# Kernel optimization log

Hardware: AMD Instinct MI355X
Metric: run time of the kernel (lower is better)

## Reference

```python
import jax, jax.numpy as jnp
import numpy as np

N = 20000      # nodes
E = 320000     # edges per metapath graph
M = 3          # metapaths
IN = 256       # input feat dim
HID = 64       # num_hidden per head
NH = 4         # nhead (layer 1)
OUT = 256      # out_dim
NHO = 1        # nhead_out (layer 2)
SA_H = 128     # semantic attention hidden
NEG_SLOPE = 0.2


def gat_conv(h, W, attn_l, attn_r, src, dst, apply_relu):
    # h: [N, F_in]; W: [F_in, H*D]; attn_l/attn_r: [H, D]
    H, D = attn_l.shape
    feat = (h @ W).reshape(N, H, D)                      # [N, H, D]
    el = jnp.sum(feat * attn_l, axis=-1)                 # [N, H]
    er = jnp.sum(feat * attn_r, axis=-1)                 # [N, H]
    e = jax.nn.leaky_relu(el[src] + er[dst], NEG_SLOPE)  # [E, H]
    # edge softmax grouped by destination node
    emax = jax.ops.segment_max(e, dst, num_segments=N)   # [N, H] (-inf for empty)
    emax = jnp.where(jnp.isfinite(emax), emax, 0.0)
    ee = jnp.exp(e - emax[dst])                          # [E, H]
    denom = jax.ops.segment_sum(ee, dst, num_segments=N) # [N, H]
    alpha = ee / (denom[dst] + 1e-9)                     # [E, H]
    msg = alpha[:, :, None] * feat[src]                  # [E, H, D]
    out = jax.ops.segment_sum(msg, dst, num_segments=N)  # [N, H, D]
    out = out.reshape(N, H * D)                          # concat heads
    return jax.nn.relu(out) if apply_relu else out


def semantic_attention(z, W1, b1, v):
    # z: [N, M, F]
    w = jnp.tanh(z @ W1 + b1) @ v          # [N, M, 1]
    w = w.mean(axis=0)                     # [M, 1]
    beta = jax.nn.softmax(w, axis=0)       # [M, 1]
    out = jnp.sum(beta[None, :, :] * z, axis=1)  # [N, F]
    att_mp = beta.squeeze()                # [M]
    return out, att_mp


def setup_inputs() -> dict:
    key = jax.random.key(0)
    ks = jax.random.split(key, 16)
    s = 0.05
    return {
        "x": jax.random.normal(ks[0], (N, IN), dtype=jnp.float32),
        "edges": jax.random.randint(ks[1], (M, 2, E), 0, N, dtype=jnp.int64)
                 if jax.config.jax_enable_x64 else
                 jax.random.randint(ks[1], (M, 2, E), 0, N, dtype=jnp.int32),
        "W1": jax.random.normal(ks[2], (IN, NH * HID), dtype=jnp.float32) * s,
        "al1": jax.random.normal(ks[3], (NH, HID), dtype=jnp.float32) * s,
        "ar1": jax.random.normal(ks[4], (NH, HID), dtype=jnp.float32) * s,
        "saW1": jax.random.normal(ks[5], (NH * HID, SA_H), dtype=jnp.float32) * s,
        "sab1": jnp.zeros((SA_H,), dtype=jnp.float32),
        "sav1": jax.random.normal(ks[6], (SA_H, 1), dtype=jnp.float32) * s,
        "W2": jax.random.normal(ks[7], (NH * HID, NHO * OUT), dtype=jnp.float32) * s,
        "al2": jax.random.normal(ks[8], (NHO, OUT), dtype=jnp.float32) * s,
        "ar2": jax.random.normal(ks[9], (NHO, OUT), dtype=jnp.float32) * s,
        "saW2": jax.random.normal(ks[10], (NHO * OUT, SA_H), dtype=jnp.float32) * s,
        "sab2": jnp.zeros((SA_H,), dtype=jnp.float32),
        "sav2": jax.random.normal(ks[11], (SA_H, 1), dtype=jnp.float32) * s,
    }


def reference(x, edges, W1, al1, ar1, saW1, sab1, sav1,
              W2, al2, ar2, saW2, sab2, sav2):
    h = x
    # HAN layer 1: shared GATConv over each metapath graph, relu activation
    z = jnp.stack([gat_conv(h, W1, al1, ar1, edges[i, 0], edges[i, 1], True)
                   for i in range(M)], axis=1)          # [N, M, NH*HID]
    h, att_mp = semantic_attention(z, saW1, sab1, sav1)
    # HAN layer 2: last layer, no activation (encoding=False)
    z = jnp.stack([gat_conv(h, W2, al2, ar2, edges[i, 0], edges[i, 1], False)
                   for i in range(M)], axis=1)          # [N, M, NHO*OUT]
    h, att_mp = semantic_attention(z, saW2, sab2, sav2)
    return h, att_mp
```

## Files before the change

### kernel.cpp

```cpp
#include <hip/hip_runtime.h>
#include <hip/hip_bf16.h>
#include <math.h>

#define NN 20000
#define EE 320000
#define MM 3
#define FW 256
#define SAH 128
#define NB 79
#define RNG 2500

typedef __attribute__((ext_vector_type(8))) short bf16x8;
typedef __attribute__((ext_vector_type(4))) float f32x4;
typedef __attribute__((ext_vector_type(2))) float f32x2;

static __device__ __forceinline__ float lrelu(float x){ return x > 0.f ? x : 0.2f*x; }

static __device__ __forceinline__ unsigned short f2bf(float f) {
    unsigned u = __float_as_uint(f);
    return (unsigned short)((u + 0x7FFFu + ((u >> 16) & 1u)) >> 16);
}
static __device__ __forceinline__ float bf2f(unsigned short b) {
    return __uint_as_float(((unsigned)b) << 16);
}
static __device__ __forceinline__ float bflo(unsigned u){ return __uint_as_float(u << 16); }
static __device__ __forceinline__ float bfhi(unsigned u){ return __uint_as_float(u & 0xffff0000u); }
static __device__ __forceinline__ unsigned pk2bf(float lo, float hi) {
    return ((unsigned)f2bf(lo)) | (((unsigned)f2bf(hi)) << 16);
}
static __device__ __forceinline__ bf16x8 u4_to_bf(uint4 u) {
    union { uint4 u; bf16x8 b; } c; c.u = u; return c.b;
}

#define ZBLK 235
__global__ __launch_bounds__(256) void prep_kernel(const float* __restrict__ W1, unsigned short* __restrict__ W1t,
                                                   const float* __restrict__ saW1, unsigned short* __restrict__ saW1t,
                                                   const float* __restrict__ W2, unsigned short* __restrict__ W2t,
                                                   const float* __restrict__ saW2, unsigned short* __restrict__ saW2t,
                                                   int* __restrict__ cnt, float* __restrict__ wsum) {
    int b2 = blockIdx.x, tid = threadIdx.x;
    if (b2 < 256)      { int n = b2;       W1t  [(size_t)n*256 + tid] = f2bf(W1  [(size_t)tid*256 + n]); return; }
    else if (b2 < 384) { int n = b2 - 256; saW1t[(size_t)n*256 + tid] = f2bf(saW1[(size_t)tid*SAH + n]); return; }
    else if (b2 < 640) { int n = b2 - 384; W2t  [(size_t)n*256 + tid] = f2bf(W2  [(size_t)tid*256 + n]); return; }
    else if (b2 < 768) { int n = b2 - 640; saW2t[(size_t)n*256 + tid] = f2bf(saW2[(size_t)tid*SAH + n]); return; }
    int zb = b2 - 768;
    int i = zb*256 + tid;
    if (i < MM*NN) cnt[i] = 0;
    if (zb == 0 && tid < 8) wsum[tid] = 0.f;
}

__global__ __launch_bounds__(256) void hist_kernel(const int* __restrict__ edges, int* __restrict__ cnt) {
    int idx = blockIdx.x*256 + threadIdx.x;
    if (idx >= MM*EE/4) return;
    int m = idx / (EE/4), e4 = idx - m*(EE/4);
    int4 d = ((const int4*)(edges + (size_t)(m*2+1)*EE))[e4];
    atomicAdd(&cnt[m*NN + d.x], 1);
    atomicAdd(&cnt[m*NN + d.y], 1);
    atomicAdd(&cnt[m*NN + d.z], 1);
    atomicAdd(&cnt[m*NN + d.w], 1);
}

__global__ __launch_bounds__(256) void scanA_kernel(const int* __restrict__ cnt, int* __restrict__ rowptr, int* __restrict__ bsum) {
    int m = blockIdx.y;
    int i = blockIdx.x*256 + threadIdx.x;
    int v = (i < NN) ? cnt[m*NN + i] : 0;
    int lane = threadIdx.x & 63;
    int val = v;
    #pragma unroll
    for (int o = 1; o < 64; o <<= 1) { int t = __shfl_up(val, o); if (lane >= o) val += t; }
    __shared__ int ws[4];
    int w = threadIdx.x >> 6;
    if (lane == 63) ws[w] = val;
    __syncthreads();
    #pragma unroll
    for (int j = 0; j < 3; ++j) if (j < w) val += ws[j];
    if (i < NN) rowptr[m*(NN+1) + 1 + i] = val;
    if (threadIdx.x == 255) bsum[m*NB + blockIdx.x] = val;
}

__global__ __launch_bounds__(128) void scanB_kernel(const int* __restrict__ bsum, int* __restrict__ boff) {
    __shared__ int s[128];
    int t = threadIdx.x;
    for (int m = 0; m < MM; ++m) {
        int v = (t < NB) ? bsum[m*NB + t] : 0;
        s[t] = v; __syncthreads();
        for (int o = 1; o < 128; o <<= 1) {
            int x = (t >= o) ? s[t - o] : 0;
            __syncthreads();
            s[t] += x;
            __syncthreads();
        }
        if (t < NB) boff[m*NB + t] = s[t] - v;
        __syncthreads();
    }
}

__global__ __launch_bounds__(256) void scanC_kernel(const int* __restrict__ cnt, int* __restrict__ rowptr,
                                                    const int* __restrict__ boff, int* __restrict__ cursor) {
    int m = blockIdx.y;
    int i = blockIdx.x*256 + threadIdx.x;
    if (i >= NN) return;
    int incl = rowptr[m*(NN+1) + 1 + i] + boff[m*NB + blockIdx.x];
    rowptr[m*(NN+1) + 1 + i] = incl;
    cursor[m*NN + i] = incl - cnt[m*NN + i];
    if (i == 0 && blockIdx.x == 0) rowptr[m*(NN+1)] = 0;
}

__global__ __launch_bounds__(256) void scatter_kernel(const int* __restrict__ edges, int* __restrict__ cursor,
                                                      int* __restrict__ csr_src) {
    int m = blockIdx.y;
    int r = blockIdx.x & 7;
    int chunk = blockIdx.x >> 3;
    int e4 = chunk*256 + threadIdx.x;
    if (e4 >= EE/4) return;
    int lo = r * RNG, hi = lo + RNG;
    int4 s = ((const int4*)(edges + (size_t)(m*2  )*EE))[e4];
    int4 d = ((const int4*)(edges + (size_t)(m*2+1)*EE))[e4];
    if (d.x >= lo && d.x < hi) { int p = atomicAdd(&cursor[m*NN + d.x], 1); csr_src[(size_t)m*EE + p] = s.x; }
    if (d.y >= lo && d.y < hi) { int p = atomicAdd(&cursor[m*NN + d.y], 1); csr_src[(size_t)m*EE + p] = s.y; }
    if (d.z >= lo && d.z < hi) { int p = atomicAdd(&cursor[m*NN + d.z], 1); csr_src[(size_t)m*EE + p] = s.z; }
    if (d.w >= lo && d.w < hi) { int p = atomicAdd(&cursor[m*NN + d.w], 1); csr_src[(size_t)m*EE + p] = s.w; }
}

template<int H, int SRC>
__global__ __launch_bounds__(256) void gemm_mfma_kernel(const float* __restrict__ Xsrc,
                                                        const unsigned short* __restrict__ Zsrc,
                                                        const float* __restrict__ wsum,
                                                        const unsigned short* __restrict__ Bt,
                                                        const float* __restrict__ attl, const float* __restrict__ attr,
                                                        unsigned short* __restrict__ C,
                                                        float* __restrict__ el, float* __restrict__ er) {
    int tid = threadIdx.x;
    int w = tid >> 6, lane = tid & 63;
    int rowgrp = w & 1, half = w >> 1;
    int r0 = blockIdx.x*32 + rowgrp*16;
    int colbase = half * 128;
    int lrow = lane & 15, lk = lane >> 4;

    __shared__ float bsh[3];
    if (SRC == 2) {
        if (tid == 0) {
            float w0 = wsum[0] / (float)NN, w1 = wsum[1] / (float)NN, w2 = wsum[2] / (float)NN;
            float mx = fmaxf(w0, fmaxf(w1, w2));
            float e0 = expf(w0 - mx), e1 = expf(w1 - mx), e2 = expf(w2 - mx);
            float s = e0 + e1 + e2;
            bsh[0] = e0 / s; bsh[1] = e1 / s; bsh[2] = e2 / s;
        }
        __syncthreads();
    }

    bf16x8 a[8];
    if (SRC == 0) {
        const float* xp = Xsrc + (size_t)(r0 + lrow)*256 + lk*8;
        #pragma unroll
        for (int k = 0; k < 8; ++k) {
            float4 v0 = *(const float4*)(xp + k*32);
            float4 v1 = *(const float4*)(xp + k*32 + 4);
            uint4 o;
            o.x = pk2bf(v0.x, v0.y); o.y = pk2bf(v0.z, v0.w);
            o.z = pk2bf(v1.x, v1.y); o.w = pk2bf(v1.z, v1.w);
            a[k] = u4_to_bf(o);
        }
    } else {
        float b0 = bsh[0], b1 = bsh[1], b2 = bsh[2];
        const unsigned short* zp = Zsrc + (size_t)(r0 + lrow)*MM*256 + lk*8;
        #pragma unroll
        for (int k = 0; k < 8; ++k) {
            uint4 z0 = *(const uint4*)(zp + k*32);
            uint4 z1 = *(const uint4*)(zp + 256 + k*32);
            uint4 z2 = *(const uint4*)(zp + 512 + k*32);
            uint4 o;
            o.x = pk2bf(b0*bflo(z0.x)+b1*bflo(z1.x)+b2*bflo(z2.x), b0*bfhi(z0.x)+b1*bfhi(z1.x)+b2*bfhi(z2.x));
            o.y = pk2bf(b0*bflo(z0.y)+b1*bflo(z1.y)+b2*bflo(z2.y), b0*bfhi(z0.y)+b1*bfhi(z1.y)+b2*bfhi(z2.y));
            o.z = pk2bf(b0*bflo(z0.z)+b1*bflo(z1.z)+b2*bflo(z2.z), b0*bfhi(z0.z)+b1*bfhi(z1.z)+b2*bfhi(z2.z));
            o.w = pk2bf(b0*bflo(z0.w)+b1*bflo(z1.w)+b2*bflo(z2.w), b0*bfhi(z0.w)+b1*bfhi(z1.w)+b2*bfhi(z2.w));
            a[k] = u4_to_bf(o);
        }
    }

    float pelv[2][4] = {{0.f,0.f,0.f,0.f},{0.f,0.f,0.f,0.f}};
    float perv[2][4] = {{0.f,0.f,0.f,0.f},{0.f,0.f,0.f,0.f}};

    #pragma unroll
    for (int n = 0; n < 8; ++n) {
        int col0 = colbase + n*16;
        const unsigned short* bp = Bt + (size_t)(col0 + lrow)*256 + lk*8;
        f32x4 acc = {0.f, 0.f, 0.f, 0.f};
        #pragma unroll
        for (int k = 0; k < 8; ++k) {
            bf16x8 bfr = *(const bf16x8*)(bp + k*32);
            acc = __builtin_amdgcn_mfma_f32_16x16x32_bf16(a[k], bfr, acc, 0, 0, 0);
        }
        int col = col0 + lrow;
        float al = attl[col], ar = attr[col];
        int hl = (H == 4) ? (n >> 2) : 0;
        #pragma unroll
        for (int r = 0; r < 4; ++r) {
            float cv = acc[r];
            pelv[hl][r] += cv * al;
            perv[hl][r] += cv * ar;
            C[(size_t)(r0 + lk*4 + r)*256 + col] = f2bf(cv);
        }
    }

    int nhl = (H == 4) ? 2 : 1;
    #pragma unroll
    for (int hl = 0; hl < 2; ++hl) {
        if (hl >= nhl) break;
        #pragma unroll
        for (int r = 0; r < 4; ++r) {
            float pe = pelv[hl][r], pr = perv[hl][r];
            #pragma unroll
            for (int o = 1; o < 16; o <<= 1) { pe += __shfl_xor(pe, o); pr += __shfl_xor(pr, o); }
            pelv[hl][r] = pe; perv[hl][r] = pr;
        }
    }

    if (H == 4) {
        if (lrow == 0) {
            int row = r0 + lk*4;
            #pragma unroll
            for (int hl = 0; hl < 2; ++hl) {
                int head = half*2 + hl;
                #pragma unroll
                for (int r = 0; r < 4; ++r) {
                    el[(size_t)(row + r)*4 + head] = pelv[hl][r];
                    er[(size_t)(row + r)*4 + head] = perv[hl][r];
                }
            }
        }
    } else {
        __shared__ float elds[2][32], erds[2][32];
        if (lrow == 0) {
            int rib = rowgrp*16 + lk*4;
            #pragma unroll
            for (int r = 0; r < 4; ++r) {
                elds[half][rib + r] = pelv[0][r];
                erds[half][rib + r] = perv[0][r];
            }
        }
        __syncthreads();
        if (tid < 32) {
            el[blockIdx.x*32 + tid] = elds[0][tid] + elds[1][tid];
            er[blockIdx.x*32 + tid] = erds[0][tid] + erds[1][tid];
        }
    }
}

template<int H>
__global__ __launch_bounds__(256) void edge_ee_kernel(const int* __restrict__ csr_src,
                                                      const int* __restrict__ rowptr,
                                                      const float* __restrict__ el, const float* __restrict__ er,
                                                      unsigned short* __restrict__ ee16) {
    int m = blockIdx.y;
    int tid = threadIdx.x;
    int g = tid >> 4, gl = tid & 15;
    int n = blockIdx.x*16 + g;
    int beg = rowptr[m*(NN+1) + n], end = rowptr[m*(NN+1) + n + 1];
    const size_t eb = (size_t)m*EE;
    if (H == 4) {
        float4 r4 = *(const float4*)&er[n*4];
        for (int e = beg + gl; e < end; e += 16) {
            int src = csr_src[eb + e];
            float4 l = *(const float4*)&el[src*4];
            uint2 o;
            o.x = pk2bf(expf(lrelu(l.x + r4.x)), expf(lrelu(l.y + r4.y)));
            o.y = pk2bf(expf(lrelu(l.z + r4.z)), expf(lrelu(l.w + r4.w)));
            *(uint2*)&ee16[(eb + e)*4] = o;
        }
    } else {
        float rn = er[n];
        for (int e = beg + gl; e < end; e += 16) {
            int src = csr_src[eb + e];
            ee16[eb + e] = f2bf(expf(lrelu(el[src] + rn)));
        }
    }
}

template<int H, bool RELU>
__global__ __launch_bounds__(256) void agg_kernel(const unsigned short* __restrict__ feat,
                                                  const unsigned short* __restrict__ ee16,
                                                  const int* __restrict__ rowptr,
                                                  const unsigned* __restrict__ csr_u,
                                                  unsigned short* __restrict__ z) {
    int m = blockIdx.y;
    int tid = threadIdx.x;
    int lane = tid & 63, wv = tid >> 6;
    int n = blockIdx.x * 4 + wv;
    int eslot = lane >> 5, flane = lane & 31;
    int h = (H == 4) ? (flane >> 3) : 0;
    int beg = rowptr[m*(NN+1) + n], end = rowptr[m*(NN+1) + n + 1];
    const size_t eb = (size_t)m*EE;

    f32x2 a2[4] = {{0.f,0.f},{0.f,0.f},{0.f,0.f},{0.f,0.f}};
    float den = 0.f;

    int e = beg + eslot;
    unsigned sA = 0, sB = 0;
    float wA = 0.f, wB = 0.f;
    if (e     < end) { sA = csr_u[eb+e  ]; wA = (H==4)? bf2f(ee16[(eb+e  )*4+h]) : bf2f(ee16[eb+e  ]); }
    if (e + 2 < end) { sB = csr_u[eb+e+2]; wB = (H==4)? bf2f(ee16[(eb+e+2)*4+h]) : bf2f(ee16[eb+e+2]); }

    while (e < end) {
        uint4 v0 = *(const uint4*)(feat + (size_t)sA*256 + flane*8);
        bool h1 = (e + 2 < end);
        uint4 v1 = make_uint4(0,0,0,0);
        if (h1) v1 = *(const uint4*)(feat + (size_t)sB*256 + flane*8);
        float w0 = wA, w1 = h1 ? wB : 0.f;
        if (e + 4 < end) { sA = csr_u[eb+e+4]; wA = (H==4)? bf2f(ee16[(eb+e+4)*4+h]) : bf2f(ee16[eb+e+4]); }
        if (e + 6 < end) { sB = csr_u[eb+e+6]; wB = (H==4)? bf2f(ee16[(eb+e+6)*4+h]) : bf2f(ee16[eb+e+6]); }
        den += w0 + w1;
        f32x2 f;
        f.x = bflo(v0.x); f.y = bfhi(v0.x); a2[0] += w0 * f;
        f.x = bflo(v0.y); f.y = bfhi(v0.y); a2[1] += w0 * f;
        f.x = bflo(v0.z); f.y = bfhi(v0.z); a2[2] += w0 * f;
        f.x = bflo(v0.w); f.y = bfhi(v0.w); a2[3] += w0 * f;
        f.x = bflo(v1.x); f.y = bfhi(v1.x); a2[0] += w1 * f;
        f.x = bflo(v1.y); f.y = bfhi(v1.y); a2[1] += w1 * f;
        f.x = bflo(v1.z); f.y = bfhi(v1.z); a2[2] += w1 * f;
        f.x = bflo(v1.w); f.y = bfhi(v1.w); a2[3] += w1 * f;
        e += 4;
    }

    #pragma unroll
    for (int j = 0; j < 4; ++j) {
        a2[j].x += __shfl_xor(a2[j].x, 32);
        a2[j].y += __shfl_xor(a2[j].y, 32);
    }
    den += __shfl_xor(den, 32);

    if (eslot == 0) {
        float inv = 1.f / (den + 1e-9f);
        #pragma unroll
        for (int j = 0; j < 4; ++j) {
            a2[j] *= inv;
            if (RELU) { a2[j].x = fmaxf(a2[j].x, 0.f); a2[j].y = fmaxf(a2[j].y, 0.f); }
        }
        uint4 pk;
        pk.x = pk2bf(a2[0].x, a2[0].y);
        pk.y = pk2bf(a2[1].x, a2[1].y);
        pk.z = pk2bf(a2[2].x, a2[2].y);
        pk.w = pk2bf(a2[3].x, a2[3].y);
        *(uint4*)&z[((size_t)n*MM + m)*256 + flane*8] = pk;
    }
}

__global__ __launch_bounds__(256) void semw_mfma_kernel(const unsigned short* __restrict__ Z,
                                                        const unsigned short* __restrict__ Wt,
                                                        const float* __restrict__ bias, const float* __restrict__ v,
                                                        float* __restrict__ wsum) {
    int tid = threadIdx.x;
    int w = tid >> 6, lane = tid & 63;
    int r0 = blockIdx.x*64 + w*16;
    int lrow = lane & 15, lk = lane >> 4;

    int arow = r0 + lrow;
    if (arow >= NN*MM) arow = NN*MM - 1;
    bf16x8 a[8];
    const unsigned short* ap = Z + (size_t)arow*256 + lk*8;
    #pragma unroll
    for (int k = 0; k < 8; ++k) a[k] = *(const bf16x8*)(ap + k*32);

    float p[4] = {0.f, 0.f, 0.f, 0.f};
    #pragma unroll
    for (int n = 0; n < 8; ++n) {
        int col = n*16 + lrow;
        const unsigned short* bp = Wt + (size_t)col*256 + lk*8;
        f32x4 acc = {0.f, 0.f, 0.f, 0.f};
        #pragma unroll
        for (int k = 0; k < 8; ++k) {
            bf16x8 bfr = *(const bf16x8*)(bp + k*32);
            acc = __builtin_amdgcn_mfma_f32_16x16x32_bf16(a[k], bfr, acc, 0, 0, 0);
        }
        float bb = bias[col], vv = v[col];
        #pragma unroll
        for (int r = 0; r < 4; ++r)
            p[r] += tanhf(acc[r] + bb) * vv;
    }

    #pragma unroll
    for (int r = 0; r < 4; ++r) {
        #pragma unroll
        for (int o = 1; o < 16; o <<= 1) p[r] += __shfl_xor(p[r], o);
    }

    __shared__ float loc[3];
    if (tid < 3) loc[tid] = 0.f;
    __syncthreads();
    if (lrow == 0) {
        #pragma unroll
        for (int r = 0; r < 4; ++r) {
            int row = r0 + lk*4 + r;
            if (row < NN*MM) atomicAdd(&loc[row % MM], p[r]);
        }
    }
    __syncthreads();
    if (tid < 3) atomicAdd(&wsum[tid], loc[tid]);
}

__global__ __launch_bounds__(128) void combine_kernel(const unsigned short* __restrict__ z, const float* __restrict__ wsum,
                                                      float* __restrict__ out, float* __restrict__ att_out) {
    __shared__ float bs[3];
    int n = blockIdx.x, t = threadIdx.x;
    if (t == 0) {
        float w0 = wsum[0] / (float)NN, w1 = wsum[1] / (float)NN, w2 = wsum[2] / (float)NN;
        float mx = fmaxf(w0, fmaxf(w1, w2));
        float e0 = expf(w0 - mx), e1 = expf(w1 - mx), e2 = expf(w2 - mx);
        float s = e0 + e1 + e2;
        bs[0] = e0 / s; bs[1] = e1 / s; bs[2] = e2 / s;
        if (n == 0) { att_out[0] = bs[0]; att_out[1] = bs[1]; att_out[2] = bs[2]; }
    }
    __syncthreads();
    float b0 = bs[0], b1 = bs[1], b2 = bs[2];
    size_t base = (size_t)n*MM*256 + t*2;
    unsigned z0 = *(const unsigned*)&z[base];
    unsigned z1 = *(const unsigned*)&z[base + 256];
    unsigned z2 = *(const unsigned*)&z[base + 512];
    float2 o;
    o.x = b0*bflo(z0) + b1*bflo(z1) + b2*bflo(z2);
    o.y = b0*bfhi(z0) + b1*bfhi(z1) + b2*bfhi(z2);
    *(float2*)&out[(size_t)n*256 + t*2] = o;
}

extern "C" void kernel_launch(void* const* d_in, const int* in_sizes, int n_in,
                              void* d_out, int out_size, void* d_ws, size_t ws_size,
                              hipStream_t stream) {
    const float* x    = (const float*)d_in[0];
    const int*   edges= (const int*)  d_in[1];
    const float* W1   = (const float*)d_in[2];
    const float* al1  = (const float*)d_in[3];
    const float* ar1  = (const float*)d_in[4];
    const float* saW1 = (const float*)d_in[5];
    const float* sab1 = (const float*)d_in[6];
    const float* sav1 = (const float*)d_in[7];
    const float* W2   = (const float*)d_in[8];
    const float* al2  = (const float*)d_in[9];
    const float* ar2  = (const float*)d_in[10];
    const float* saW2 = (const float*)d_in[11];
    const float* sab2 = (const float*)d_in[12];
    const float* sav2 = (const float*)d_in[13];
    float* out = (float*)d_out;

    char* ws = (char*)d_ws;
    size_t off = 0;
    auto alloc = [&](size_t bytes) { void* p = ws + off; off += (bytes + 255) & ~(size_t)255; return p; };
    unsigned short* feat  = (unsigned short*)alloc((size_t)NN*256*2);
    unsigned short* z     = (unsigned short*)alloc((size_t)NN*MM*256*2);
    unsigned short* W1t   = (unsigned short*)alloc(256*256*2);
    unsigned short* saW1t = (unsigned short*)alloc(SAH*256*2);
    unsigned short* W2t   = (unsigned short*)alloc(256*256*2);
    unsigned short* saW2t = (unsigned short*)alloc(SAH*256*2);
    unsigned short* ee16  = (unsigned short*)alloc((size_t)MM*EE*4*2);
    float* el     = (float*)alloc(NN*4*4);
    float* er     = (float*)alloc(NN*4*4);
    float* wsum   = (float*)alloc(256);
    int*   cnt    = (int*)alloc(MM*NN*4);
    int*   cursor = (int*)alloc(MM*NN*4);
    int*   rowptr = (int*)alloc(MM*(NN+1)*4);
    int*   csr_s  = (int*)alloc((size_t)MM*EE*4);
    int*   bsum   = (int*)alloc(MM*NB*4);
    int*   boff   = (int*)alloc(MM*NB*4);

    int egrid4 = (MM*EE/4 + 255)/256;
    int chunks = (EE/4 + 255)/256;
    dim3 sg(NB, MM);

    prep_kernel<<<768 + ZBLK, 256, 0, stream>>>(W1, W1t, saW1, saW1t, W2, W2t, saW2, saW2t, cnt, wsum);

    hist_kernel<<<egrid4, 256, 0, stream>>>(edges, cnt);
    scanA_kernel<<<sg, 256, 0, stream>>>(cnt, rowptr, bsum);
    scanB_kernel<<<1, 128, 0, stream>>>(bsum, boff);
    scanC_kernel<<<sg, 256, 0, stream>>>(cnt, rowptr, boff, cursor);
    scatter_kernel<<<dim3(chunks*8, MM), 256, 0, stream>>>(edges, cursor, csr_s);

    gemm_mfma_kernel<4, 0><<<NN/32, 256, 0, stream>>>(x, nullptr, nullptr, W1t, al1, ar1, feat, el, er);
    edge_ee_kernel<4><<<dim3(NN/16, MM), 256, 0, stream>>>(csr_s, rowptr, el, er, ee16);
    agg_kernel<4, true><<<dim3(NN/4, MM), 256, 0, stream>>>(feat, ee16, rowptr, (const unsigned*)csr_s, z);
    semw_mfma_kernel<<<(NN*MM + 63)/64, 256, 0, stream>>>(z, saW1t, sab1, sav1, wsum);

    gemm_mfma_kernel<1, 2><<<NN/32, 256, 0, stream>>>(nullptr, z, wsum, W2t, al2, ar2, feat, el, er);
    edge_ee_kernel<1><<<dim3(NN/16, MM), 256, 0, stream>>>(csr_s, rowptr, el, er, ee16);
    agg_kernel<1, false><<<dim3(NN/4, MM), 256, 0, stream>>>(feat, ee16, rowptr, (const unsigned*)csr_s, z);
    semw_mfma_kernel<<<(NN*MM + 63)/64, 256, 0, stream>>>(z, saW2t, sab2, sav2, wsum + 4);
    combine_kernel<<<NN, 128, 0, stream>>>(z, wsum + 4, out, out + (size_t)NN*256);
}
```

Before: 392.3 us.

## Fuse edge exp-score computation into aggregation kernel via per-wave LDS staging

Removes the separate edge_ee kernels and the bf16 ee16 buffer. Each wave now computes the exp(leaky_relu(el+er)) weights for its node's incoming edges into shared memory, then runs aggregation. Nodes with degree above a cap recompute the weights inline. This saves two launches and a global write/read of edge weights, at the cost of extra LDS use and a block-wide sync in the aggregation kernel.

```diff
diff --git a/kernel.cpp b/kernel.cpp
--- a/kernel.cpp
+++ b/kernel.cpp
@@ -9,6 +9,7 @@
 #define SAH 128
 #define NB 79
 #define RNG 2500
+#define DCAP 192
 
 typedef __attribute__((ext_vector_type(8))) short bf16x8;
 typedef __attribute__((ext_vector_type(4))) float f32x4;
@@ -19,9 +20,6 @@
 static __device__ __forceinline__ unsigned short f2bf(float f) {
     unsigned u = __float_as_uint(f);
     return (unsigned short)((u + 0x7FFFu + ((u >> 16) & 1u)) >> 16);
-}
-static __device__ __forceinline__ float bf2f(unsigned short b) {
-    return __uint_as_float(((unsigned)b) << 16);
 }
 static __device__ __forceinline__ float bflo(unsigned u){ return __uint_as_float(u << 16); }
 static __device__ __forceinline__ float bfhi(unsigned u){ return __uint_as_float(u & 0xffff0000u); }
@@ -247,42 +245,16 @@
     }
 }
 
-template<int H>
-__global__ __launch_bounds__(256) void edge_ee_kernel(const int* __restrict__ csr_src,
-                                                      const int* __restrict__ rowptr,
-                                                      const float* __restrict__ el, const float* __restrict__ er,
-                                                      unsigned short* __restrict__ ee16) {
-    int m = blockIdx.y;
-    int tid = threadIdx.x;
-    int g = tid >> 4, gl = tid & 15;
-    int n = blockIdx.x*16 + g;
-    int beg = rowptr[m*(NN+1) + n], end = rowptr[m*(NN+1) + n + 1];
-    const size_t eb = (size_t)m*EE;
-    if (H == 4) {
-        float4 r4 = *(const float4*)&er[n*4];
-        for (int e = beg + gl; e < end; e += 16) {
-            int src = csr_src[eb + e];
-            float4 l = *(const float4*)&el[src*4];
-            uint2 o;
-            o.x = pk2bf(expf(lrelu(l.x + r4.x)), expf(lrelu(l.y + r4.y)));
-            o.y = pk2bf(expf(lrelu(l.z + r4.z)), expf(lrelu(l.w + r4.w)));
-            *(uint2*)&ee16[(eb + e)*4] = o;
-        }
-    } else {
-        float rn = er[n];
-        for (int e = beg + gl; e < end; e += 16) {
-            int src = csr_src[eb + e];
-            ee16[eb + e] = f2bf(expf(lrelu(el[src] + rn)));
-        }
-    }
-}
-
 template<int H, bool RELU>
 __global__ __launch_bounds__(256) void agg_kernel(const unsigned short* __restrict__ feat,
-                                                  const unsigned short* __restrict__ ee16,
+                                                  const float* __restrict__ el,
+                                                  const float* __restrict__ er,
                                                   const int* __restrict__ rowptr,
                                                   const unsigned* __restrict__ csr_u,
                                                   unsigned short* __restrict__ z) {
+    constexpr int EW = (H == 4) ? 4 : 1;
+    __shared__ float eelds[4][DCAP*EW];
+
     int m = blockIdx.y;
     int tid = threadIdx.x;
     int lane = tid & 63, wv = tid >> 6;
@@ -290,25 +262,61 @@
     int eslot = lane >> 5, flane = lane & 31;
     int h = (H == 4) ? (flane >> 3) : 0;
     int beg = rowptr[m*(NN+1) + n], end = rowptr[m*(NN+1) + n + 1];
+    int deg = end - beg;
+    bool ovf = deg > DCAP;
     const size_t eb = (size_t)m*EE;
+
+    if (!ovf) {
+        if (H == 4) {
+            float4 r4 = *(const float4*)&er[n*4];
+            for (int i = lane; i < deg; i += 64) {
+                int src = csr_u[eb + beg + i];
+                float4 l = *(const float4*)&el[src*4];
+                float4 o;
+                o.x = expf(lrelu(l.x + r4.x));
+                o.y = expf(lrelu(l.y + r4.y));
+                o.z = expf(lrelu(l.z + r4.z));
+                o.w = expf(lrelu(l.w + r4.w));
+                *(float4*)&eelds[wv][i*4] = o;
+            }
+        } else {
+            float rn = er[n];
+            for (int i = lane; i < deg; i += 64) {
+                int src = csr_u[eb + beg + i];
+                eelds[wv][i] = expf(lrelu(el[src] + rn));
+            }
+        }
+    }
+    __syncthreads();
+
+    float ern = 0.f;
+    if (ovf) ern = (H == 4) ? er[n*4 + h] : er[n];
 
     f32x2 a2[4] = {{0.f,0.f},{0.f,0.f},{0.f,0.f},{0.f,0.f}};
     float den = 0.f;
 
     int e = beg + eslot;
     unsigned sA = 0, sB = 0;
-    float wA = 0.f, wB = 0.f;
-    if (e     < end) { sA = csr_u[eb+e  ]; wA = (H==4)? bf2f(ee16[(eb+e  )*4+h]) : bf2f(ee16[eb+e  ]); }
-    if (e + 2 < end) { sB = csr_u[eb+e+2]; wB = (H==4)? bf2f(ee16[(eb+e+2)*4+h]) : bf2f(ee16[eb+e+2]); }
+    if (e     < end) sA = csr_u[eb+e  ];
+    if (e + 2 < end) sB = csr_u[eb+e+2];
 
     while (e < end) {
         uint4 v0 = *(const uint4*)(feat + (size_t)sA*256 + flane*8);
         bool h1 = (e + 2 < end);
         uint4 v1 = make_uint4(0,0,0,0);
         if (h1) v1 = *(const uint4*)(feat + (size_t)sB*256 + flane*8);
-        float w0 = wA, w1 = h1 ? wB : 0.f;
-        if (e + 4 < end) { sA = csr_u[eb+e+4]; wA = (H==4)? bf2f(ee16[(eb+e+4)*4+h]) : bf2f(ee16[eb+e+4]); }
-        if (e + 6 < end) { sB = csr_u[eb+e+6]; wB = (H==4)? bf2f(ee16[(eb+e+6)*4+h]) : bf2f(ee16[eb+e+6]); }
+        float w0, w1;
+        if (!ovf) {
+            w0 = eelds[wv][(e - beg)*EW + ((H==4)?h:0)];
+            w1 = h1 ? eelds[wv][(e + 2 - beg)*EW + ((H==4)?h:0)] : 0.f;
+        } else {
+            float lA = (H==4)? el[sA*4+h] : el[sA];
+            float lB = h1 ? ((H==4)? el[sB*4+h] : el[sB]) : 0.f;
+            w0 = expf(lrelu(lA + ern));
+            w1 = h1 ? expf(lrelu(lB + ern)) : 0.f;
+        }
+        if (e + 4 < end) sA = csr_u[eb+e+4];
+        if (e + 6 < end) sB = csr_u[eb+e+6];
         den += w0 + w1;
         f32x2 f;
         f.x = bflo(v0.x); f.y = bfhi(v0.x); a2[0] += w0 * f;
@@ -450,7 +458,6 @@
     unsigned short* saW1t = (unsigned short*)alloc(SAH*256*2);
     unsigned short* W2t   = (unsigned short*)alloc(256*256*2);
     unsigned short* saW2t = (unsigned short*)alloc(SAH*256*2);
-    unsigned short* ee16  = (unsigned short*)alloc((size_t)MM*EE*4*2);
     float* el     = (float*)alloc(NN*4*4);
     float* er     = (float*)alloc(NN*4*4);
     float* wsum   = (float*)alloc(256);
@@ -474,13 +481,11 @@
     scatter_kernel<<<dim3(chunks*8, MM), 256, 0, stream>>>(edges, cursor, csr_s);
 
     gemm_mfma_kernel<4, 0><<<NN/32, 256, 0, stream>>>(x, nullptr, nullptr, W1t, al1, ar1, feat, el, er);
-    edge_ee_kernel<4><<<dim3(NN/16, MM), 256, 0, stream>>>(csr_s, rowptr, el, er, ee16);
-    agg_kernel<4, true><<<dim3(NN/4, MM), 256, 0, stream>>>(feat, ee16, rowptr, (const unsigned*)csr_s, z);
+    agg_kernel<4, true><<<dim3(NN/4, MM), 256, 0, stream>>>(feat, el, er, rowptr, (const unsigned*)csr_s, z);
     semw_mfma_kernel<<<(NN*MM + 63)/64, 256, 0, stream>>>(z, saW1t, sab1, sav1, wsum);
 
     gemm_mfma_kernel<1, 2><<<NN/32, 256, 0, stream>>>(nullptr, z, wsum, W2t, al2, ar2, feat, el, er);
-    edge_ee_kernel<1><<<dim3(NN/16, MM), 256, 0, stream>>>(csr_s, rowptr, el, er, ee16);
-    agg_kernel<1, false><<<dim3(NN/4, MM), 256, 0, stream>>>(feat, ee16, rowptr, (const unsigned*)csr_s, z);
+    agg_kernel<1, false><<<dim3(NN/4, MM), 256, 0, stream>>>(feat, el, er, rowptr, (const unsigned*)csr_s, z);
     semw_mfma_kernel<<<(NN*MM + 63)/64, 256, 0, stream>>>(z, saW2t, sab2, sav2, wsum + 4);
     combine_kernel<<<NN, 128, 0, stream>>>(z, wsum + 4, out, out + (size_t)NN*256);
 }
```

After: 396.7 us. About the same (+1.1%).
